# Performance work log

Hardware: AMD Instinct MI355X
Metric: run time of the kernel (lower is better)

Reference implementation:

```python
import jax, jax.numpy as jnp
import numpy as np

NUM_CODEBOOKS = 4
CODEBOOK_SIZE = 4096
CODEBOOK_DIM = 512


def setup_inputs() -> dict:
    key = jax.random.key(0)
    k1, k2 = jax.random.split(key)
    inputs = jax.random.normal(k1, (8, 2048, CODEBOOK_DIM), dtype=jnp.float32)
    # nn.init.uniform_(codebook.weight, -1/codebook_size, 1/codebook_size)
    bound = 1.0 / CODEBOOK_SIZE
    codebook = jax.random.uniform(k2, (CODEBOOK_SIZE, CODEBOOK_DIM),
                                  dtype=jnp.float32, minval=-bound, maxval=bound)
    return {"inputs": inputs, "codebook": codebook}


def reference(inputs, codebook):
    original_shape = inputs.shape
    x = inputs.reshape(-1, CODEBOOK_DIM)  # [N, D]
    cb_sq = jnp.sum(codebook ** 2, axis=1)  # [K]

    def stage(residual, _):
        # distances: ||r||^2 - 2 r.W^T + ||w||^2  -> [N, K]
        distances = (jnp.sum(residual ** 2, axis=1, keepdims=True)
                     - 2.0 * residual @ codebook.T
                     + cb_sq[None, :])
        indices = jnp.argmin(distances, axis=-1)  # [N]
        # one-hot matmul in torch == gather; same math
        quantized = codebook[indices]  # [N, D]
        # straight-through estimator
        q_ste = residual + jax.lax.stop_gradient(quantized - residual)
        new_residual = residual - q_ste
        return new_residual, (q_ste, indices)

    _, (q_stages, idx_stages) = jax.lax.scan(stage, x, None, length=NUM_CODEBOOKS)
    quantized_out = jnp.sum(q_stages, axis=0).reshape(original_shape)
    # all_indices stacked along last dim: [B, T, num_codebooks]
    all_indices = jnp.moveaxis(idx_stages, 0, -1).reshape(*original_shape[:-1], NUM_CODEBOOKS)
    vq_loss = jnp.float32(0.0)  # eval mode: self.training is False
    return quantized_out, all_indices, vq_loss
```

## Files before the change

kernel.cpp:

```cpp
#include <hip/hip_runtime.h>
#include <math.h>


namespace {
constexpr int N_ROWS     = 16384;
constexpr int DIM        = 512;
constexpr int K_CODES    = 4096;
constexpr int NUM_STAGES = 4;

constexpr int KTILES = 32;
constexpr float EPS  = 1e-3f;
constexpr int CAP    = 2;

constexpr size_t Q_OFF    = 0;
constexpr size_t IDX_OFF  = (size_t)N_ROWS * DIM;
constexpr size_t LOSS_OFF = IDX_OFF + (size_t)N_ROWS * NUM_STAGES;

constexpr size_t RES_OFF  = 0;
constexpr size_t RH_OFF   = (size_t)N_ROWS * DIM * 4;
constexpr size_t WH_OFF   = RH_OFF + (size_t)N_ROWS * DIM * 2;
constexpr size_t CBSQ_OFF = WH_OFF + (size_t)K_CODES * DIM * 2;
constexpr size_t RSQ_OFF  = CBSQ_OFF + (size_t)K_CODES * 4;
constexpr size_t PART_OFF = RSQ_OFF + (size_t)N_ROWS * 4;
constexpr size_t GBUF_OFF = PART_OFF + (size_t)N_ROWS * KTILES * 4;

constexpr unsigned long long EMPTY_E = 0xFFFFFFFFFFFFFFFFull;
constexpr unsigned long long OVFL_E  = 0xFFFFFFFFFFFFFFFEull;
}

typedef short bf16x8 __attribute__((ext_vector_type(8)));
typedef float f32x4  __attribute__((ext_vector_type(4)));

typedef __attribute__((address_space(1))) const unsigned int glob_u32;
typedef __attribute__((address_space(3))) unsigned int lds_u32;

__device__ __forceinline__ unsigned short f2bf(float x) {
    unsigned int u = __float_as_uint(x);
    return (unsigned short)((u + 0x7fffu + ((u >> 16) & 1u)) >> 16);
}

__device__ __forceinline__ float rowsq_tree(const float v8[8], int lane) {
#pragma clang fp contract(off)
    float P[4];
#pragma unroll
    for (int b = 0; b < 4; ++b) {
        float xa = v8[2 * b];
        float xb = v8[2 * b + 1];
        float sa = xa * xa;
        float sb = xb * xb;
        float R  = sa + sb;
        float t  = R + __shfl_down(R, 16, 64);
        float u  = t + __shfl_down(t, 32, 64);
        float a  = u + __shfl_down(u, 8, 64);
        float c  = a + __shfl_down(a, 4, 64);
        float d  = c + __shfl_down(c, 2, 64);
        P[b]     = d + __shfl_down(d, 1, 64);
    }
    float s01 = P[0] + P[1];
    float s23 = P[2] + P[3];
    return s01 + s23;
}

__global__ __launch_bounds__(64)
void cbsq_wh_kernel(const float* __restrict__ cb, float* __restrict__ cb_sq,
                    unsigned short* __restrict__ wh, float* __restrict__ loss) {
    int k = blockIdx.x;
    int lane = threadIdx.x;
    const float* row = cb + (size_t)k * DIM;
    unsigned short* whp = wh + (size_t)k * DIM;
    float v8[8];
#pragma unroll
    for (int i = 0; i < 8; ++i) {
        float v = row[lane + i * 64];
        v8[i] = v;
        whp[lane + i * 64] = f2bf(v);
    }
    float s = rowsq_tree(v8, lane);
    if (lane == 0) cb_sq[k] = s;
    if (k == 0 && lane == 0) *loss = 0.0f;
}

__global__ __launch_bounds__(256)
void init_kernel(const float* __restrict__ input,
                 unsigned short* __restrict__ rh,
                 float* __restrict__ rsq) {
    const int t = threadIdx.x;
    const int lane = t & 63;
    const int sub  = t >> 6;
    const int row  = blockIdx.x * 4 + sub;
    const float* x = input + (size_t)row * DIM;
    unsigned short* rhp = rh + (size_t)row * DIM;
    float v8[8];
#pragma unroll
    for (int i = 0; i < 8; ++i) {
        int d = lane + i * 64;
        float v = x[d];
        v8[i] = v;
        rhp[d] = f2bf(v);
    }
    float s = rowsq_tree(v8, lane);
    if (lane == 0) rsq[row] = s;
}

__global__ __launch_bounds__(256, 2)
void passA_kernel(const unsigned short* __restrict__ rh,
                  const unsigned short* __restrict__ wh,
                  const float* __restrict__ cb_sq,
                  const float* __restrict__ rsq,
                  float* __restrict__ part,
                  unsigned long long* __restrict__ gbuf) {
    const int lin = blockIdx.x + KTILES * blockIdx.y;
    const int xcd = lin & 7;
    const int c   = lin >> 3;
    const int jb  = c & 31;
    const int mb  = xcd * 16 + (c >> 5);
    const int mbase = mb * 128;
    const int nbase = jb * 128;

    __shared__ __align__(16) unsigned short At[128 * 64];
    __shared__ __align__(16) unsigned short Bt[128 * 64];
    __shared__ float rowmin[128][2];

    const int t    = threadIdx.x;
    const int lane = t & 63;
    const int wid  = t >> 6;
    const int wr   = wid >> 1;
    const int wc   = wid & 1;

    const int lrow = lane >> 3;
    const int d8g  = (lane & 7) ^ lrow;

    f32x4 acc[4][4];
#pragma unroll
    for (int mi = 0; mi < 4; ++mi)
#pragma unroll
        for (int ni = 0; ni < 4; ++ni) acc[mi][ni] = (f32x4){0.f, 0.f, 0.f, 0.f};

    for (int k0 = 0; k0 < DIM; k0 += 64) {
#pragma unroll
        for (int i = 0; i < 4; ++i) {
            int rbase = wid * 32 + i * 8;
            int grow  = rbase + lrow;
            const unsigned short* ga =
                rh + (size_t)(mbase + grow) * DIM + k0 + d8g * 8;
            __builtin_amdgcn_global_load_lds(
                (glob_u32*)ga, (lds_u32*)&At[rbase * 64], 16, 0, 0);
            const unsigned short* gb =
                wh + (size_t)(nbase + grow) * DIM + k0 + d8g * 8;
            __builtin_amdgcn_global_load_lds(
                (glob_u32*)gb, (lds_u32*)&Bt[rbase * 64], 16, 0, 0);
        }
        __syncthreads();

#pragma unroll
        for (int kk = 0; kk < 2; ++kk) {
            bf16x8 af[4], bfr[4];
            const int g = kk * 4 + (lane >> 4);
#pragma unroll
            for (int mi = 0; mi < 4; ++mi) {
                int row = wr * 64 + mi * 16 + (lane & 15);
                af[mi] = *(const bf16x8*)&At[row * 64 + (g ^ (row & 7)) * 8];
            }
#pragma unroll
            for (int ni = 0; ni < 4; ++ni) {
                int row = wc * 64 + ni * 16 + (lane & 15);
                bfr[ni] = *(const bf16x8*)&Bt[row * 64 + (g ^ (row & 7)) * 8];
            }
#pragma unroll
            for (int mi = 0; mi < 4; ++mi)
#pragma unroll
                for (int ni = 0; ni < 4; ++ni)
                    acc[mi][ni] = __builtin_amdgcn_mfma_f32_16x16x32_bf16(
                        af[mi], bfr[ni], acc[mi][ni], 0, 0, 0);
        }
        __syncthreads();
    }

    int* scnt = (int*)Bt;
    unsigned long long* sbuf = (unsigned long long*)At;
    if (t < 128) {
        scnt[t] = 0;
        sbuf[t * CAP + 0] = EMPTY_E;
        sbuf[t * CAP + 1] = EMPTY_E;
    }

#pragma unroll
    for (int mi = 0; mi < 4; ++mi) {
#pragma unroll
        for (int reg = 0; reg < 4; ++reg) {
            int rloc = wr * 64 + mi * 16 + (lane >> 4) * 4 + reg;
            float rsqv = rsq[mbase + rloc];
            float m = INFINITY;
#pragma unroll
            for (int ni = 0; ni < 4; ++ni) {
                int kg = nbase + wc * 64 + ni * 16 + (lane & 15);
                float y;
                {
#pragma clang fp contract(off)
                    float t2 = 2.0f * acc[mi][ni][reg];
                    float u  = rsqv - t2;
                    y        = u + cb_sq[kg];
                }
                m = fminf(m, y);
            }
#pragma unroll
            for (int off = 1; off < 16; off <<= 1)
                m = fminf(m, __shfl_xor(m, off, 64));
            if ((lane & 15) == 0) rowmin[rloc][wc] = m;
        }
    }
    __syncthreads();

#pragma unroll
    for (int mi = 0; mi < 4; ++mi) {
#pragma unroll
        for (int reg = 0; reg < 4; ++reg) {
            int rloc = wr * 64 + mi * 16 + (lane >> 4) * 4 + reg;
            float thrT = fminf(rowmin[rloc][0], rowmin[rloc][1]) + EPS;
            float rsqv = rsq[mbase + rloc];
#pragma unroll
            for (int ni = 0; ni < 4; ++ni) {
                int kg = nbase + wc * 64 + ni * 16 + (lane & 15);
                float y;
                {
#pragma clang fp contract(off)
                    float t2 = 2.0f * acc[mi][ni][reg];
                    float u  = rsqv - t2;
                    y        = u + cb_sq[kg];
                }
                if (y <= thrT) {
                    int pos = atomicAdd(&scnt[rloc], 1);
                    if (pos < CAP)
                        sbuf[rloc * CAP + pos] =
                            ((unsigned long long)__float_as_uint(y) << 32) |
                            (unsigned)kg;
                }
            }
        }
    }
    __syncthreads();

    if (t < 128) {
        part[(size_t)jb * N_ROWS + (mbase + t)] =
            fminf(rowmin[t][0], rowmin[t][1]);
        unsigned long long s0 = sbuf[t * CAP + 0];
        unsigned long long s1 = sbuf[t * CAP + 1];
        if (scnt[t] > CAP) s0 = OVFL_E;
        size_t bidx = ((size_t)jb * N_ROWS + (mbase + t)) * CAP;
        gbuf[bidx]     = s0;
        gbuf[bidx + 1] = s1;
    }
}

__global__ __launch_bounds__(256)
void finish_kernel(float* __restrict__ res,
                   const float* __restrict__ rin,
                   const float* __restrict__ cb,
                   const float* __restrict__ cb_sq,
                   float* __restrict__ rsq,
                   const float* __restrict__ part,
                   const unsigned long long* __restrict__ gbuf,
                   float* __restrict__ qout,
                   float* __restrict__ idx_out,
                   unsigned short* __restrict__ rh,
                   int stage, int do_next) {
#pragma clang fp contract(off)
    const int t   = threadIdx.x;
    const int jr  = t & 31;
    const int rs  = t >> 5;
    const int row = blockIdx.x * 8 + rs;

    float pv = part[(size_t)jr * N_ROWS + row];
    float m = pv;
#pragma unroll
    for (int off = 1; off < 32; off <<= 1)
        m = fminf(m, __shfl_xor(m, off, 32));
    const float thr = m + EPS;

    unsigned long long s0 = EMPTY_E, s1 = EMPTY_E;
    bool surv = (pv <= thr);
    if (surv) {
        size_t bidx = ((size_t)jr * N_ROWS + row) * CAP;
        s0 = gbuf[bidx];
        s1 = gbuf[bidx + 1];
    }
    const bool ovfl = surv && (s0 == OVFL_E);

    int lcl = 0;
    unsigned long long cand = EMPTY_E;
    float y0 = __uint_as_float((unsigned)(s0 >> 32));
    float y1 = __uint_as_float((unsigned)(s1 >> 32));
    if (surv && !ovfl) {
        if (y0 <= thr) { lcl++; cand = s0; }
        if (y1 <= thr) { lcl++; cand = s1; }
    }
    int tot = lcl;
    int oc  = ovfl ? 1 : 0;
#pragma unroll
    for (int off = 1; off < 32; off <<= 1) {
        tot += __shfl_xor(tot, off, 32);
        oc  += __shfl_xor(oc, off, 32);
    }

    const float* rr  = rin + (size_t)row * DIM;
    const float rsqv = rsq[row];

    unsigned long long lpk;
    if (tot == 1 && oc == 0) {
        lpk = (lcl == 1) ? cand : EMPTY_E;
    } else {
        float by = INFINITY; int bk = 0x7fffffff;
        if (surv && !ovfl && lcl > 0) {
#pragma unroll
            for (int sl = 0; sl < CAP; ++sl) {
                unsigned long long s = sl ? s1 : s0;
                float yh = __uint_as_float((unsigned)(s >> 32));
                if (!(yh <= thr)) continue;
                int k = (int)(s & 0xFFFFFFFFull);
                const float* wp = cb + (size_t)k * DIM;
                float dot = 0.0f;
#pragma unroll 8
                for (int d = 0; d < DIM; d += 4) {
                    float4 r4 = *(const float4*)(rr + d);
                    float4 w4 = *(const float4*)(wp + d);
                    dot = fmaf(r4.x, w4.x, dot);
                    dot = fmaf(r4.y, w4.y, dot);
                    dot = fmaf(r4.z, w4.z, dot);
                    dot = fmaf(r4.w, w4.w, dot);
                }
                float t2 = 2.0f * dot;
                float u  = rsqv - t2;
                float y  = u + cb_sq[k];
                if (y < by || (y == by && k < bk)) { by = y; bk = k; }
            }
        }
        unsigned grp = (unsigned)(__ballot(ovfl) >> (t & 32));
        while (grp) {
            int jt = __builtin_ctz(grp);
            grp &= grp - 1;
#pragma unroll
            for (int q = 0; q < 4; ++q) {
                int k = jt * 128 + jr * 4 + q;
                const float* wp = cb + (size_t)k * DIM;
                float dot = 0.0f;
#pragma unroll 8
                for (int d = 0; d < DIM; d += 4) {
                    float4 r4 = *(const float4*)(rr + d);
                    float4 w4 = *(const float4*)(wp + d);
                    dot = fmaf(r4.x, w4.x, dot);
                    dot = fmaf(r4.y, w4.y, dot);
                    dot = fmaf(r4.z, w4.z, dot);
                    dot = fmaf(r4.w, w4.w, dot);
                }
                float t2 = 2.0f * dot;
                float u  = rsqv - t2;
                float y  = u + cb_sq[k];
                if (y < by || (y == by && k < bk)) { by = y; bk = k; }
            }
        }
        lpk = ((unsigned long long)__float_as_uint(by) << 32) | (unsigned)bk;
    }

#pragma unroll
    for (int off = 1; off < 32; off <<= 1) {
        unsigned long long o =
            (unsigned long long)__shfl_xor((long long)lpk, off, 32);
        if (o < lpk) lpk = o;
    }
    const int bi = (int)(lpk & 0xFFFFFFFFull);
    if (jr == 0) idx_out[(size_t)row * NUM_STAGES + stage] = (float)bi;

    const float* wp = cb + (size_t)bi * DIM;
    float*       rp = res + (size_t)row * DIM;
    float*       qp = qout + (size_t)row * DIM;
    unsigned short* rhp = rh + (size_t)row * DIM;

    float4 rn4[4];
#pragma unroll
    for (int i = 0; i < 4; ++i) {
        int d0 = 4 * jr + 128 * i;
        float4 wv = *(const float4*)(wp + d0);
        float4 rv = *(const float4*)(rr + d0);
        float4 qs, rn;
        qs.x = rv.x + (wv.x - rv.x);  rn.x = rv.x - qs.x;
        qs.y = rv.y + (wv.y - rv.y);  rn.y = rv.y - qs.y;
        qs.z = rv.z + (wv.z - rv.z);  rn.z = rv.z - qs.z;
        qs.w = rv.w + (wv.w - rv.w);  rn.w = rv.w - qs.w;
        rn4[i] = rn;
        if (do_next) {
            *(float4*)(rp + d0) = rn;
            ushort4 h;
            h.x = f2bf(rn.x); h.y = f2bf(rn.y);
            h.z = f2bf(rn.z); h.w = f2bf(rn.w);
            *(ushort4*)(rhp + d0) = h;
        }
        if (stage == 0) {
            *(float4*)(qp + d0) = qs;
        } else {
            float4 qo = *(const float4*)(qp + d0);
            qo.x = qo.x + qs.x; qo.y = qo.y + qs.y;
            qo.z = qo.z + qs.z; qo.w = qo.w + qs.w;
            *(float4*)(qp + d0) = qo;
        }
    }

    if (do_next) {
        float P[4];
#pragma unroll
        for (int b = 0; b < 4; ++b) {
            float4 v = rn4[b];
            float sqx = v.x * v.x, sqy = v.y * v.y;
            float sqz = v.z * v.z, sqw = v.w * v.w;
            float Rx = sqx + __shfl_down(sqx, 16, 32);
            float Ry = sqy + __shfl_down(sqy, 16, 32);
            float Rz = sqz + __shfl_down(sqz, 16, 32);
            float Rw = sqw + __shfl_down(sqw, 16, 32);
            float tx = Rx + __shfl_down(Rx, 4, 32);
            float ty = Ry + __shfl_down(Ry, 4, 32);
            float tz = Rz + __shfl_down(Rz, 4, 32);
            float tw = Rw + __shfl_down(Rw, 4, 32);
            float ux = tx + __shfl_down(tx, 8, 32);
            float uy = ty + __shfl_down(ty, 8, 32);
            float uz = tz + __shfl_down(tz, 8, 32);
            float uw = tw + __shfl_down(tw, 8, 32);
            float ax = ux + __shfl_down(ux, 2, 32);
            float ay = uy + __shfl_down(uy, 2, 32);
            float az = uz + __shfl_down(uz, 2, 32);
            float aw = uw + __shfl_down(uw, 2, 32);
            float cx = ax + __shfl_down(ax, 1, 32);
            float cy = ay + __shfl_down(ay, 1, 32);
            float cz = az + __shfl_down(az, 1, 32);
            float cw = aw + __shfl_down(aw, 1, 32);
            float d0 = cx + cz;
            float d1 = cy + cw;
            P[b] = d0 + d1;
        }
        float s01 = P[0] + P[1];
        float s23 = P[2] + P[3];
        if (jr == 0) rsq[row] = s01 + s23;
    }
}

extern "C" void kernel_launch(void* const* d_in, const int* in_sizes, int n_in,
                              void* d_out, int out_size, void* d_ws, size_t ws_size,
                              hipStream_t stream) {
    const float* input = (const float*)d_in[0];
    const float* cb    = (const float*)d_in[1];

    float* out_f   = (float*)d_out;
    float* qout    = out_f + Q_OFF;
    float* idx_out = out_f + IDX_OFF;
    float* loss    = out_f + LOSS_OFF;

    char* ws = (char*)d_ws;
    float*          residual = (float*)(ws + RES_OFF);
    unsigned short* rh       = (unsigned short*)(ws + RH_OFF);
    unsigned short* wh       = (unsigned short*)(ws + WH_OFF);
    float*          cb_sq    = (float*)(ws + CBSQ_OFF);
    float*          rsq      = (float*)(ws + RSQ_OFF);
    float*          part     = (float*)(ws + PART_OFF);
    unsigned long long* gbuf = (unsigned long long*)(ws + GBUF_OFF);

    cbsq_wh_kernel<<<K_CODES, 64, 0, stream>>>(cb, cb_sq, wh, loss);
    init_kernel<<<N_ROWS / 4, 256, 0, stream>>>(input, rh, rsq);

    for (int s = 0; s < NUM_STAGES; ++s) {
        const float* rin = (s == 0) ? input : residual;
        passA_kernel<<<dim3(KTILES, N_ROWS / 128), 256, 0, stream>>>(
            rh, wh, cb_sq, rsq, part, gbuf);
        finish_kernel<<<N_ROWS / 8, 256, 0, stream>>>(
            residual, rin, cb, cb_sq, rsq, part, gbuf,
            qout, idx_out, rh, s, (s < NUM_STAGES - 1) ? 1 : 0);
    }
}
```

Baseline: 851.0 us.

## Merge setup kernels and stage finish-kernel part/gbuf loads through shared memory

Merges the codebook prep and input prep kernels into a single setup launch, which saves one kernel launch. The finish kernel now handles 32 rows per block in four iterations. Each iteration loads the part and gbuf entries with coalesced row-contiguous reads into shared memory, then reads them back transposed. The residual row is prefetched into registers and reused in the update, replacing a second global read. The costs are extra __syncthreads, fewer blocks per finish launch, and the risk that gbuf is not 16-byte aligned for the ulonglong2 loads.

```diff
diff --git a/kernel.cpp b/kernel.cpp
--- a/kernel.cpp
+++ b/kernel.cpp
@@ -11,6 +11,8 @@
 constexpr int KTILES = 32;
 constexpr float EPS  = 1e-3f;
 constexpr int CAP    = 2;
+
+constexpr int FROWS  = 32;
 
 constexpr size_t Q_OFF    = 0;
 constexpr size_t IDX_OFF  = (size_t)N_ROWS * DIM;
@@ -61,45 +63,43 @@
     return s01 + s23;
 }
 
-__global__ __launch_bounds__(64)
-void cbsq_wh_kernel(const float* __restrict__ cb, float* __restrict__ cb_sq,
-                    unsigned short* __restrict__ wh, float* __restrict__ loss) {
-    int k = blockIdx.x;
-    int lane = threadIdx.x;
-    const float* row = cb + (size_t)k * DIM;
-    unsigned short* whp = wh + (size_t)k * DIM;
-    float v8[8];
-#pragma unroll
-    for (int i = 0; i < 8; ++i) {
-        float v = row[lane + i * 64];
-        v8[i] = v;
-        whp[lane + i * 64] = f2bf(v);
-    }
-    float s = rowsq_tree(v8, lane);
-    if (lane == 0) cb_sq[k] = s;
-    if (k == 0 && lane == 0) *loss = 0.0f;
-}
-
 __global__ __launch_bounds__(256)
-void init_kernel(const float* __restrict__ input,
-                 unsigned short* __restrict__ rh,
-                 float* __restrict__ rsq) {
-    const int t = threadIdx.x;
+void setup_kernel(const float* __restrict__ cb, float* __restrict__ cb_sq,
+                  unsigned short* __restrict__ wh, float* __restrict__ loss,
+                  const float* __restrict__ input,
+                  unsigned short* __restrict__ rh, float* __restrict__ rsq) {
+    const int t    = threadIdx.x;
     const int lane = t & 63;
     const int sub  = t >> 6;
-    const int row  = blockIdx.x * 4 + sub;
-    const float* x = input + (size_t)row * DIM;
-    unsigned short* rhp = rh + (size_t)row * DIM;
-    float v8[8];
-#pragma unroll
-    for (int i = 0; i < 8; ++i) {
-        int d = lane + i * 64;
-        float v = x[d];
-        v8[i] = v;
-        rhp[d] = f2bf(v);
-    }
-    float s = rowsq_tree(v8, lane);
-    if (lane == 0) rsq[row] = s;
+    if (blockIdx.x < 1024) {
+        int k = blockIdx.x * 4 + sub;
+        const float* row = cb + (size_t)k * DIM;
+        unsigned short* whp = wh + (size_t)k * DIM;
+        float v8[8];
+#pragma unroll
+        for (int i = 0; i < 8; ++i) {
+            float v = row[lane + i * 64];
+            v8[i] = v;
+            whp[lane + i * 64] = f2bf(v);
+        }
+        float s = rowsq_tree(v8, lane);
+        if (lane == 0) cb_sq[k] = s;
+        if (k == 0 && lane == 0) *loss = 0.0f;
+    } else {
+        int row = (blockIdx.x - 1024) * 4 + sub;
+        const float* x = input + (size_t)row * DIM;
+        unsigned short* rhp = rh + (size_t)row * DIM;
+        float v8[8];
+#pragma unroll
+        for (int i = 0; i < 8; ++i) {
+            int d = lane + i * 64;
+            float v = x[d];
+            v8[i] = v;
+            rhp[d] = f2bf(v);
+        }
+        float s = rowsq_tree(v8, lane);
+        if (lane == 0) rsq[row] = s;
+    }
 }
 
 __global__ __launch_bounds__(256, 2)
@@ -265,179 +265,197 @@
                    unsigned short* __restrict__ rh,
                    int stage, int do_next) {
 #pragma clang fp contract(off)
-    const int t   = threadIdx.x;
-    const int jr  = t & 31;
-    const int rs  = t >> 5;
-    const int row = blockIdx.x * 8 + rs;
-
-    float pv = part[(size_t)jr * N_ROWS + row];
-    float m = pv;
-#pragma unroll
-    for (int off = 1; off < 32; off <<= 1)
-        m = fminf(m, __shfl_xor(m, off, 32));
-    const float thr = m + EPS;
-
-    unsigned long long s0 = EMPTY_E, s1 = EMPTY_E;
-    bool surv = (pv <= thr);
-    if (surv) {
-        size_t bidx = ((size_t)jr * N_ROWS + row) * CAP;
-        s0 = gbuf[bidx];
-        s1 = gbuf[bidx + 1];
-    }
-    const bool ovfl = surv && (s0 == OVFL_E);
-
-    int lcl = 0;
-    unsigned long long cand = EMPTY_E;
-    float y0 = __uint_as_float((unsigned)(s0 >> 32));
-    float y1 = __uint_as_float((unsigned)(s1 >> 32));
-    if (surv && !ovfl) {
-        if (y0 <= thr) { lcl++; cand = s0; }
-        if (y1 <= thr) { lcl++; cand = s1; }
-    }
-    int tot = lcl;
-    int oc  = ovfl ? 1 : 0;
-#pragma unroll
-    for (int off = 1; off < 32; off <<= 1) {
-        tot += __shfl_xor(tot, off, 32);
-        oc  += __shfl_xor(oc, off, 32);
-    }
-
-    const float* rr  = rin + (size_t)row * DIM;
-    const float rsqv = rsq[row];
-
-    unsigned long long lpk;
-    if (tot == 1 && oc == 0) {
-        lpk = (lcl == 1) ? cand : EMPTY_E;
-    } else {
-        float by = INFINITY; int bk = 0x7fffffff;
-        if (surv && !ovfl && lcl > 0) {
-#pragma unroll
-            for (int sl = 0; sl < CAP; ++sl) {
-                unsigned long long s = sl ? s1 : s0;
-                float yh = __uint_as_float((unsigned)(s >> 32));
-                if (!(yh <= thr)) continue;
-                int k = (int)(s & 0xFFFFFFFFull);
-                const float* wp = cb + (size_t)k * DIM;
-                float dot = 0.0f;
+    const int t  = threadIdx.x;
+    const int jr = t & 31;
+    const int rs = t >> 5;
+    const int jr_l = t >> 3;
+    const int ro   = t & 7;
+
+    __shared__ float partS[256];
+    __shared__ ulonglong2 gbufS[256];
+
+    for (int it = 0; it < FROWS / 8; ++it) {
+        const int row0 = blockIdx.x * FROWS + it * 8;
+        const int row  = row0 + rs;
+
+        __syncthreads();
+        partS[jr_l * 8 + ro] = part[(size_t)jr_l * N_ROWS + row0 + ro];
+        gbufS[jr_l * 8 + ro] =
+            *(const ulonglong2*)&gbuf[((size_t)jr_l * N_ROWS + row0 + ro) * CAP];
+
+        const float* rr = rin + (size_t)row * DIM;
+        float4 rv4[4];
+#pragma unroll
+        for (int i = 0; i < 4; ++i)
+            rv4[i] = *(const float4*)(rr + 4 * jr + 128 * i);
+
+        __syncthreads();
+
+        float pv = partS[jr * 8 + rs];
+        float m = pv;
+#pragma unroll
+        for (int off = 1; off < 32; off <<= 1)
+            m = fminf(m, __shfl_xor(m, off, 32));
+        const float thr = m + EPS;
+
+        ulonglong2 sv = gbufS[jr * 8 + rs];
+        unsigned long long s0 = sv.x, s1 = sv.y;
+        bool surv = (pv <= thr);
+        if (!surv) { s0 = EMPTY_E; s1 = EMPTY_E; }
+        const bool ovfl = surv && (s0 == OVFL_E);
+
+        int lcl = 0;
+        unsigned long long cand = EMPTY_E;
+        float y0 = __uint_as_float((unsigned)(s0 >> 32));
+        float y1 = __uint_as_float((unsigned)(s1 >> 32));
+        if (surv && !ovfl) {
+            if (y0 <= thr) { lcl++; cand = s0; }
+            if (y1 <= thr) { lcl++; cand = s1; }
+        }
+        int tot = lcl;
+        int oc  = ovfl ? 1 : 0;
+#pragma unroll
+        for (int off = 1; off < 32; off <<= 1) {
+            tot += __shfl_xor(tot, off, 32);
+            oc  += __shfl_xor(oc, off, 32);
+        }
+
+        const float rsqv = rsq[row];
+
+        unsigned long long lpk;
+        if (tot == 1 && oc == 0) {
+            lpk = (lcl == 1) ? cand : EMPTY_E;
+        } else {
+            float by = INFINITY; int bk = 0x7fffffff;
+            if (surv && !ovfl && lcl > 0) {
+#pragma unroll
+                for (int sl = 0; sl < CAP; ++sl) {
+                    unsigned long long s = sl ? s1 : s0;
+                    float yh = __uint_as_float((unsigned)(s >> 32));
+                    if (!(yh <= thr)) continue;
+                    int k = (int)(s & 0xFFFFFFFFull);
+                    const float* wp = cb + (size_t)k * DIM;
+                    float dot = 0.0f;
 #pragma unroll 8
-                for (int d = 0; d < DIM; d += 4) {
-                    float4 r4 = *(const float4*)(rr + d);
-                    float4 w4 = *(const float4*)(wp + d);
-                    dot = fmaf(r4.x, w4.x, dot);
-                    dot = fmaf(r4.y, w4.y, dot);
-                    dot = fmaf(r4.z, w4.z, dot);
-                    dot = fmaf(r4.w, w4.w, dot);
+                    for (int d = 0; d < DIM; d += 4) {
+                        float4 r4 = *(const float4*)(rr + d);
+                        float4 w4 = *(const float4*)(wp + d);
+                        dot = fmaf(r4.x, w4.x, dot);
+                        dot = fmaf(r4.y, w4.y, dot);
+                        dot = fmaf(r4.z, w4.z, dot);
+                        dot = fmaf(r4.w, w4.w, dot);
+                    }
+                    float t2 = 2.0f * dot;
+                    float u  = rsqv - t2;
+                    float y  = u + cb_sq[k];
+                    if (y < by || (y == by && k < bk)) { by = y; bk = k; }
                 }
-                float t2 = 2.0f * dot;
-                float u  = rsqv - t2;
-                float y  = u + cb_sq[k];
-                if (y < by || (y == by && k < bk)) { by = y; bk = k; }
-            }
-        }
-        unsigned grp = (unsigned)(__ballot(ovfl) >> (t & 32));
-        while (grp) {
-            int jt = __builtin_ctz(grp);
-            grp &= grp - 1;
-#pragma unroll
-            for (int q = 0; q < 4; ++q) {
-                int k = jt * 128 + jr * 4 + q;
-                const float* wp = cb + (size_t)k * DIM;
-                float dot = 0.0f;
+            }
+            unsigned grp = (unsigned)(__ballot(ovfl) >> (t & 32));
+            while (grp) {
+                int jt = __builtin_ctz(grp);
+                grp &= grp - 1;
+#pragma unroll
+                for (int q = 0; q < 4; ++q) {
+                    int k = jt * 128 + jr * 4 + q;
+                    const float* wp = cb + (size_t)k * DIM;
+                    float dot = 0.0f;
 #pragma unroll 8
-                for (int d = 0; d < DIM; d += 4) {
-                    float4 r4 = *(const float4*)(rr + d);
-                    float4 w4 = *(const float4*)(wp + d);
-                    dot = fmaf(r4.x, w4.x, dot);
-                    dot = fmaf(r4.y, w4.y, dot);
-                    dot = fmaf(r4.z, w4.z, dot);
-                    dot = fmaf(r4.w, w4.w, dot);
+                    for (int d = 0; d < DIM; d += 4) {
+                        float4 r4 = *(const float4*)(rr + d);
+                        float4 w4 = *(const float4*)(wp + d);
+                        dot = fmaf(r4.x, w4.x, dot);
+                        dot = fmaf(r4.y, w4.y, dot);
+                        dot = fmaf(r4.z, w4.z, dot);
+                        dot = fmaf(r4.w, w4.w, dot);
+                    }
+                    float t2 = 2.0f * dot;
+                    float u  = rsqv - t2;
+                    float y  = u + cb_sq[k];
+                    if (y < by || (y == by && k < bk)) { by = y; bk = k; }
                 }
-                float t2 = 2.0f * dot;
-                float u  = rsqv - t2;
-                float y  = u + cb_sq[k];
-                if (y < by || (y == by && k < bk)) { by = y; bk = k; }
-            }
-        }
-        lpk = ((unsigned long long)__float_as_uint(by) << 32) | (unsigned)bk;
-    }
-
-#pragma unroll
-    for (int off = 1; off < 32; off <<= 1) {
-        unsigned long long o =
-            (unsigned long long)__shfl_xor((long long)lpk, off, 32);
-        if (o < lpk) lpk = o;
-    }
-    const int bi = (int)(lpk & 0xFFFFFFFFull);
-    if (jr == 0) idx_out[(size_t)row * NUM_STAGES + stage] = (float)bi;
-
-    const float* wp = cb + (size_t)bi * DIM;
-    float*       rp = res + (size_t)row * DIM;
-    float*       qp = qout + (size_t)row * DIM;
-    unsigned short* rhp = rh + (size_t)row * DIM;
-
-    float4 rn4[4];
-#pragma unroll
-    for (int i = 0; i < 4; ++i) {
-        int d0 = 4 * jr + 128 * i;
-        float4 wv = *(const float4*)(wp + d0);
-        float4 rv = *(const float4*)(rr + d0);
-        float4 qs, rn;
-        qs.x = rv.x + (wv.x - rv.x);  rn.x = rv.x - qs.x;
-        qs.y = rv.y + (wv.y - rv.y);  rn.y = rv.y - qs.y;
-        qs.z = rv.z + (wv.z - rv.z);  rn.z = rv.z - qs.z;
-        qs.w = rv.w + (wv.w - rv.w);  rn.w = rv.w - qs.w;
-        rn4[i] = rn;
+            }
+            lpk = ((unsigned long long)__float_as_uint(by) << 32) | (unsigned)bk;
+        }
+
+#pragma unroll
+        for (int off = 1; off < 32; off <<= 1) {
+            unsigned long long o =
+                (unsigned long long)__shfl_xor((long long)lpk, off, 32);
+            if (o < lpk) lpk = o;
+        }
+        const int bi = (int)(lpk & 0xFFFFFFFFull);
+        if (jr == 0) idx_out[(size_t)row * NUM_STAGES + stage] = (float)bi;
+
+        const float* wp = cb + (size_t)bi * DIM;
+        float*       rp = res + (size_t)row * DIM;
+        float*       qp = qout + (size_t)row * DIM;
+        unsigned short* rhp = rh + (size_t)row * DIM;
+
+        float4 rn4[4];
+#pragma unroll
+        for (int i = 0; i < 4; ++i) {
+            int d0 = 4 * jr + 128 * i;
+            float4 wv = *(const float4*)(wp + d0);
+            float4 rv = rv4[i];
+            float4 qs, rn;
+            qs.x = rv.x + (wv.x - rv.x);  rn.x = rv.x - qs.x;
+            qs.y = rv.y + (wv.y - rv.y);  rn.y = rv.y - qs.y;
+            qs.z = rv.z + (wv.z - rv.z);  rn.z = rv.z - qs.z;
+            qs.w = rv.w + (wv.w - rv.w);  rn.w = rv.w - qs.w;
+            rn4[i] = rn;
+            if (do_next) {
+                *(float4*)(rp + d0) = rn;
+                ushort4 h;
+                h.x = f2bf(rn.x); h.y = f2bf(rn.y);
+                h.z = f2bf(rn.z); h.w = f2bf(rn.w);
+                *(ushort4*)(rhp + d0) = h;
+            }
+            if (stage == 0) {
+                *(float4*)(qp + d0) = qs;
+            } else {
+                float4 qo = *(const float4*)(qp + d0);
+                qo.x = qo.x + qs.x; qo.y = qo.y + qs.y;
+                qo.z = qo.z + qs.z; qo.w = qo.w + qs.w;
+                *(float4*)(qp + d0) = qo;
+            }
+        }
+
         if (do_next) {
-            *(float4*)(rp + d0) = rn;
-            ushort4 h;
-            h.x = f2bf(rn.x); h.y = f2bf(rn.y);
-            h.z = f2bf(rn.z); h.w = f2bf(rn.w);
-            *(ushort4*)(rhp + d0) = h;
-        }
-        if (stage == 0) {
-            *(float4*)(qp + d0) = qs;
-        } else {
-            float4 qo = *(const float4*)(qp + d0);
-            qo.x = qo.x + qs.x; qo.y = qo.y + qs.y;
-            qo.z = qo.z + qs.z; qo.w = qo.w + qs.w;
-            *(float4*)(qp + d0) = qo;
-        }
-    }
-
-    if (do_next) {
-        float P[4];
-#pragma unroll
-        for (int b = 0; b < 4; ++b) {
-            float4 v = rn4[b];
-            float sqx = v.x * v.x, sqy = v.y * v.y;
-            float sqz = v.z * v.z, sqw = v.w * v.w;
-            float Rx = sqx + __shfl_down(sqx, 16, 32);
-            float Ry = sqy + __shfl_down(sqy, 16, 32);
-            float Rz = sqz + __shfl_down(sqz, 16, 32);
-            float Rw = sqw + __shfl_down(sqw, 16, 32);
-            float tx = Rx + __shfl_down(Rx, 4, 32);
-            float ty = Ry + __shfl_down(Ry, 4, 32);
-            float tz = Rz + __shfl_down(Rz, 4, 32);
-            float tw = Rw + __shfl_down(Rw, 4, 32);
-            float ux = tx + __shfl_down(tx, 8, 32);
-            float uy = ty + __shfl_down(ty, 8, 32);
-            float uz = tz + __shfl_down(tz, 8, 32);
-            float uw = tw + __shfl_down(tw, 8, 32);
-            float ax = ux + __shfl_down(ux, 2, 32);
-            float ay = uy + __shfl_down(uy, 2, 32);
-            float az = uz + __shfl_down(uz, 2, 32);
-            float aw = uw + __shfl_down(uw, 2, 32);
-            float cx = ax + __shfl_down(ax, 1, 32);
-            float cy = ay + __shfl_down(ay, 1, 32);
-            float cz = az + __shfl_down(az, 1, 32);
-            float cw = aw + __shfl_down(aw, 1, 32);
-            float d0 = cx + cz;
-            float d1 = cy + cw;
-            P[b] = d0 + d1;
-        }
-        float s01 = P[0] + P[1];
-        float s23 = P[2] + P[3];
-        if (jr == 0) rsq[row] = s01 + s23;
+            float P[4];
+#pragma unroll
+            for (int b = 0; b < 4; ++b) {
+                float4 v = rn4[b];
+                float sqx = v.x * v.x, sqy = v.y * v.y;
+                float sqz = v.z * v.z, sqw = v.w * v.w;
+                float Rx = sqx + __shfl_down(sqx, 16, 32);
+                float Ry = sqy + __shfl_down(sqy, 16, 32);
+                float Rz = sqz + __shfl_down(sqz, 16, 32);
+                float Rw = sqw + __shfl_down(sqw, 16, 32);
+                float tx = Rx + __shfl_down(Rx, 4, 32);
+                float ty = Ry + __shfl_down(Ry, 4, 32);
+                float tz = Rz + __shfl_down(Rz, 4, 32);
+                float tw = Rw + __shfl_down(Rw, 4, 32);
+                float ux = tx + __shfl_down(tx, 8, 32);
+                float uy = ty + __shfl_down(ty, 8, 32);
+                float uz = tz + __shfl_down(tz, 8, 32);
+                float uw = tw + __shfl_down(tw, 8, 32);
+                float ax = ux + __shfl_down(ux, 2, 32);
+                float ay = uy + __shfl_down(uy, 2, 32);
+                float az = uz + __shfl_down(uz, 2, 32);
+                float aw = uw + __shfl_down(uw, 2, 32);
+                float cx = ax + __shfl_down(ax, 1, 32);
+                float cy = ay + __shfl_down(ay, 1, 32);
+                float cz = az + __shfl_down(az, 1, 32);
+                float cw = aw + __shfl_down(aw, 1, 32);
+                float d0 = cx + cz;
+                float d1 = cy + cw;
+                P[b] = d0 + d1;
+            }
+            float s01 = P[0] + P[1];
+            float s23 = P[2] + P[3];
+            if (jr == 0) rsq[row] = s01 + s23;
+        }
     }
 }
 
@@ -461,14 +479,14 @@
     float*          part     = (float*)(ws + PART_OFF);
     unsigned long long* gbuf = (unsigned long long*)(ws + GBUF_OFF);
 
-    cbsq_wh_kernel<<<K_CODES, 64, 0, stream>>>(cb, cb_sq, wh, loss);
-    init_kernel<<<N_ROWS / 4, 256, 0, stream>>>(input, rh, rsq);
+    setup_kernel<<<1024 + N_ROWS / 4, 256, 0, stream>>>(
+        cb, cb_sq, wh, loss, input, rh, rsq);
 
     for (int s = 0; s < NUM_STAGES; ++s) {
         const float* rin = (s == 0) ? input : residual;
         passA_kernel<<<dim3(KTILES, N_ROWS / 128), 256, 0, stream>>>(
             rh, wh, cb_sq, rsq, part, gbuf);
-        finish_kernel<<<N_ROWS / 8, 256, 0, stream>>>(
+        finish_kernel<<<N_ROWS / FROWS, 256, 0, stream>>>(
             residual, rin, cb, cb_sq, rsq, part, gbuf,
             qout, idx_out, rh, s, (s < NUM_STAGES - 1) ? 1 : 0);
     }
```

New measurement: 948.2 us. 1.11x slower.
